# Kernel optimization log

Measured on AMD Instinct MI355X. Metric: run time of the kernel, lower is better.

Reference implementation:

```python
import jax, jax.numpy as jnp
import numpy as np

DOWN = 4
FOCAL_A, FOCAL_B = 2.0, 4.0
RAD_ALPHA = 0.54
HM_W, WH_W = 1.0, 0.1
B, NUM_CLASSES, H, W = 16, 80, 128, 128
MAX_OBJ, N_VALID = 100, 60


def setup_inputs() -> dict:
    key = jax.random.key(0)
    k1, k2, k3, k4, k5, k6, k7, k8 = jax.random.split(key, 8)
    heatmap_heads = jax.random.normal(k1, (B, NUM_CLASSES, H, W), dtype=jnp.float32)
    # wh heads are non-negative distances (l,t,r,b) in input-image pixels
    wh_heads = jax.random.uniform(k2, (B, 4, H, W), dtype=jnp.float32) * 32.0
    # synthetic COCO-style annotations: (x1,y1,x2,y2,cls), cls=-1 pads
    x1 = jax.random.uniform(k3, (B, MAX_OBJ)) * 400.0
    y1 = jax.random.uniform(k4, (B, MAX_OBJ)) * 400.0
    bw = 16.0 + jax.random.uniform(k5, (B, MAX_OBJ)) * 96.0
    bh = 16.0 + jax.random.uniform(k6, (B, MAX_OBJ)) * 96.0
    x2 = jnp.minimum(x1 + bw, 511.0)
    y2 = jnp.minimum(y1 + bh, 511.0)
    cls = jax.random.randint(k7, (B, MAX_OBJ), 0, NUM_CLASSES).astype(jnp.float32)
    cls = jnp.where(jnp.arange(MAX_OBJ)[None, :] < N_VALID, cls, -1.0)
    annotations = jnp.stack([x1, y1, x2, y2, cls], axis=-1).astype(jnp.float32)
    return {"heatmap_heads": heatmap_heads, "wh_heads": wh_heads, "annotations": annotations}


def _single_targets(annots, num_classes, height, width):
    # annots: [N,5]; replicates TTFNet per-image target generation, vectorized.
    boxes = annots[:, :4]
    cls = annots[:, 4]
    valid = cls >= 0
    areas = (boxes[:, 3] - boxes[:, 1] + 1.0) * (boxes[:, 2] - boxes[:, 0] + 1.0)
    log_a = jnp.where(valid, jnp.log(jnp.maximum(areas, 1e-12)), -jnp.inf)
    order = jnp.argsort(-log_a)
    boxes, cls, valid = boxes[order], cls[order], valid[order]
    cx = jnp.trunc((boxes[:, 0] + boxes[:, 2]) * 0.5 / DOWN)
    cy = jnp.trunc((boxes[:, 1] + boxes[:, 3]) * 0.5 / DOWN)
    fx1 = jnp.clip(boxes[:, 0] / DOWN, 0.0, width - 1)
    fx2 = jnp.clip(boxes[:, 2] / DOWN, 0.0, width - 1)
    fy1 = jnp.clip(boxes[:, 1] / DOWN, 0.0, height - 1)
    fy2 = jnp.clip(boxes[:, 3] / DOWN, 0.0, height - 1)
    hr = ((fy2 - fy1) * 0.5 * RAD_ALPHA).astype(jnp.int32)  # .int() trunc (coords >= 0)
    wr = ((fx2 - fx1) * 0.5 * RAD_ALPHA).astype(jnp.int32)
    sx = (2 * wr + 1).astype(jnp.float32) / 6.0  # sigma_x = w/6
    sy = (2 * hr + 1).astype(jnp.float32) / 6.0  # sigma_y = h/6
    xs = jnp.arange(width, dtype=jnp.float32)
    ys = jnp.arange(height, dtype=jnp.float32)
    dx = xs[None, :] - cx[:, None]  # [N,W]
    dy = ys[None, :] - cy[:, None]  # [N,H]
    gx = jnp.where((jnp.abs(dx) <= wr[:, None]) & valid[:, None],
                   jnp.exp(-(dx * dx) / (2.0 * sx[:, None] * sx[:, None])), 0.0)
    gy = jnp.where(jnp.abs(dy) <= hr[:, None],
                   jnp.exp(-(dy * dy) / (2.0 * sy[:, None] * sy[:, None])), 0.0)
    g = gy[:, :, None] * gx[:, None, :]  # [N,H,W] truncated gaussian per box
    cls_idx = jnp.clip(cls.astype(jnp.int32), 0, num_classes - 1)
    hm = jnp.zeros((num_classes, height, width), jnp.float32).at[cls_idx].max(g)
    n = g.shape[0]
    idx = jnp.arange(n)[:, None, None]
    owner = jnp.max(jnp.where(g > 0, idx, -1), axis=0)  # last (smallest) box covering each pixel
    covered = owner >= 0
    oc = jnp.clip(owner, 0)
    box_t = jnp.where(covered[None], jnp.transpose(boxes[oc], (2, 0, 1)), -1.0)  # [4,H,W]
    gsum = jnp.maximum(g.sum(axis=(1, 2)), 1e-12)
    wnorm = g / gsum[:, None, None]  # local_heatmap / ct_div (boxes_area_topk_log is forced to 1.0)
    reg = jnp.where(covered, jnp.take_along_axis(wnorm, oc[None], axis=0)[0], 0.0)[None]  # [1,H,W]
    return hm, box_t, reg


def _forward(heatmap_heads, wh_heads, annotations):
    b, num_classes, height, width = heatmap_heads.shape
    hm_t, box_t, reg_w = jax.vmap(lambda a: _single_targets(a, num_classes, height, width))(annotations)
    hm_t = jax.lax.stop_gradient(hm_t)
    box_t = jax.lax.stop_gradient(box_t)
    reg_w = jax.lax.stop_gradient(reg_w)

    pred = jax.nn.sigmoid(heatmap_heads).transpose(0, 2, 3, 1).reshape(b, -1, num_classes)
    wh = wh_heads.transpose(0, 2, 3, 1).reshape(b, -1, 4)
    tgt = hm_t.transpose(0, 2, 3, 1).reshape(b, -1, num_classes)
    boxes = box_t.transpose(0, 2, 3, 1).reshape(b, -1, 4)
    w = reg_w.transpose(0, 2, 3, 1).reshape(b, -1)

    # focal (CornerNet-style) heatmap loss
    pos = (tgt == 1.0).astype(jnp.float32)
    neg = (tgt < 1.0).astype(jnp.float32)
    neg_wt = (1.0 - tgt) ** FOCAL_B
    pos_loss = jnp.sum(-jnp.log(pred) * (1.0 - pred) ** FOCAL_A * pos)
    neg_loss = jnp.sum(-jnp.log(1.0 - pred) * pred ** FOCAL_A * neg_wt * neg)
    num_pos = pos.sum()
    hm_loss = jnp.where(num_pos > 0, (pos_loss + neg_loss) / num_pos, neg_loss) * HM_W

    # decode predicted boxes on feature grid (stride = down_ratio)
    shift_y, shift_x = jnp.meshgrid(jnp.arange(height, dtype=jnp.float32) * DOWN,
                                    jnp.arange(width, dtype=jnp.float32) * DOWN, indexing='ij')
    base = jnp.stack([shift_x, shift_y], axis=-1).reshape(-1, 2)  # [HW,2]
    pred_boxes = jnp.concatenate([base[None] - wh[:, :, :2], base[None] + wh[:, :, 2:]], axis=2)

    avg_factor = w.sum() + 1e-4
    m = w > 0
    safe = jnp.array([0.0, 0.0, 1.0, 1.0], jnp.float32)
    p = jnp.where(m[..., None], pred_boxes, safe)
    t = jnp.where(m[..., None], boxes, safe)
    lt = jnp.maximum(p[..., :2], t[..., :2])
    rb = jnp.minimum(p[..., 2:], t[..., 2:])
    wh_i = jnp.clip(rb - lt + 1.0, 0.0)
    e1 = jnp.minimum(p[..., :2], t[..., :2])
    e2 = jnp.maximum(p[..., 2:], t[..., 2:])
    ewh = jnp.clip(e2 - e1 + 1.0, 0.0)
    overlap = wh_i[..., 0] * wh_i[..., 1]
    ap = (p[..., 2] - p[..., 0] + 1.0) * (p[..., 3] - p[..., 1] + 1.0)
    ag = (t[..., 2] - t[..., 0] + 1.0) * (t[..., 3] - t[..., 1] + 1.0)
    u = ap + ag - overlap
    ious = overlap / u
    e_area = ewh[..., 0] * ewh[..., 1]
    gious = ious - (e_area - u) / e_area
    wh_loss = (jnp.sum((1.0 - gious) * w) / avg_factor)[None] * WH_W
    return hm_loss, wh_loss


def reference(heatmap_heads, wh_heads, annotations):
    return _forward(heatmap_heads, wh_heads, annotations)
```

## Files before the change

kernel.cpp:

```cpp
#include <hip/hip_runtime.h>
#include <math.h>

#define NB 16
#define NC 80
#define HH 128
#define WW 128
#define NOBJ 100
#define HW (HH*WW)
#define DENSE_BLOCKS 1280
#define TOTAL_BLOCKS (DENSE_BLOCKS + NB*NOBJ)

enum { P_CX=0, P_CY, P_WR, P_HR, P_IVX, P_IVY, P_IVG, P_X1, P_Y1, P_X2, P_Y2, P_CLS, NPAR };

#define ACC_DOUBLES 96
#define NV_OFF 768
#define PAR_OFF 832

__global__ __launch_bounds__(128) void prep_kernel(const float* __restrict__ ann,
                                                   double* __restrict__ acc,
                                                   int* __restrict__ nv,
                                                   float* __restrict__ par) {
    int b = blockIdx.x;
    int i = threadIdx.x;
    __shared__ float skey[128];
    __shared__ int s_nv;
    if (i == 0) s_nv = 0;

    if (i < 5) acc[i * 16 + b] = 0.0;
    if (i == 5) acc[80 + b] = 0.0;

    float x1=0.f, y1=0.f, x2=0.f, y2=0.f, clsv=-1.f;
    float key = INFINITY;
    if (i < NOBJ) {
        const float* a = ann + ((size_t)b * NOBJ + i) * 5;
        x1=a[0]; y1=a[1]; x2=a[2]; y2=a[3]; clsv=a[4];
        if (clsv >= 0.f) {
            float area = (y2 - y1 + 1.f) * (x2 - x1 + 1.f);
            key = -__logf(fmaxf(area, 1e-12f));
        }
    }
    skey[i] = key;
    __syncthreads();

    if (i < NOBJ) {
        int r = 0;
        for (int j = 0; j < NOBJ; ++j) {
            float kj = skey[j];
            if (kj < key || (kj == key && j < i)) r++;
        }
        bool valid = (clsv >= 0.f);
        if (valid) atomicAdd(&s_nv, 1);

        float cx = truncf((x1 + x2) * 0.125f);
        float cy = truncf((y1 + y2) * 0.125f);
        float fx1 = fminf(fmaxf(x1*0.25f, 0.f), WW - 1.f);
        float fx2 = fminf(fmaxf(x2*0.25f, 0.f), WW - 1.f);
        float fy1 = fminf(fmaxf(y1*0.25f, 0.f), HH - 1.f);
        float fy2 = fminf(fmaxf(y2*0.25f, 0.f), HH - 1.f);
        int hr = (int)((fy2 - fy1) * 0.5f * 0.54f);
        int wr = (int)((fx2 - fx1) * 0.5f * 0.54f);
        float sx = (float)(2*wr + 1) / 6.0f;
        float sy = (float)(2*hr + 1) / 6.0f;
        float ivx = 1.f / (2.f * sx * sx);
        float ivy = 1.f / (2.f * sy * sy);

        int yc = (int)cy, xc = (int)cx;
        float sgy = 0.f;
        {
            int ya = max(0, yc - hr), yb = min(HH - 1, yc + hr);
            for (int y = ya; y <= yb; ++y) {
                float dy = (float)y - cy;
                sgy += __expf(-(dy*dy) * ivy);
            }
        }
        float sgx = 0.f;
        if (valid) {
            int xa = max(0, xc - wr), xb = min(WW - 1, xc + wr);
            for (int x = xa; x <= xb; ++x) {
                float dx = (float)x - cx;
                sgx += __expf(-(dx*dx) * ivx);
            }
        }
        float gsum = fmaxf(sgy * sgx, 1e-12f);
        int cls_i = min(max((int)clsv, 0), NC - 1);

        size_t o = (size_t)b * NOBJ + (size_t)r;
        size_t S = (size_t)NB * NOBJ;
        par[P_CX*S + o]  = cx;
        par[P_CY*S + o]  = cy;
        par[P_WR*S + o]  = (float)wr;
        par[P_HR*S + o]  = (float)hr;
        par[P_IVX*S + o] = ivx;
        par[P_IVY*S + o] = ivy;
        par[P_IVG*S + o] = 1.f / gsum;
        par[P_X1*S + o]  = x1;
        par[P_Y1*S + o]  = y1;
        par[P_X2*S + o]  = x2;
        par[P_Y2*S + o]  = y2;
        par[P_CLS*S + o] = __int_as_float(cls_i);
    }
    __syncthreads();
    if (i == 0) nv[b] = s_nv;
}

__global__ __launch_bounds__(256) void main_kernel(const float* __restrict__ heat,
                                                   const float* __restrict__ wh,
                                                   const float* __restrict__ par,
                                                   const int* __restrict__ nv,
                                                   double* __restrict__ acc) {
    if (blockIdx.x < DENSE_BLOCKS) {
        const float4* hp = (const float4*)heat;
        size_t base = (size_t)blockIdx.x * 4096 + threadIdx.x;
        float4 v[16];
        #pragma unroll
        for (int k = 0; k < 16; ++k) v[k] = hp[base + (size_t)k * 256];
        float negl = 0.f;
        #pragma unroll
        for (int k = 0; k < 16; ++k) {
            float hv[4] = { v[k].x, v[k].y, v[k].z, v[k].w };
            #pragma unroll
            for (int m = 0; m < 4; ++m) {
                float h = hv[m];
                float e = __expf(-h);
                float q = 1.f + e;
                float lq = __logf(q);
                float p = 1.f / q;
                negl += (h + lq) * p * p;
            }
        }
        float r = negl;
        for (int off = 32; off > 0; off >>= 1) r += __shfl_down(r, off, 64);
        __shared__ float dred[4];
        int lane = threadIdx.x & 63, wv = threadIdx.x >> 6;
        if (lane == 0) dred[wv] = r;
        __syncthreads();
        if (threadIdx.x == 0) {
            double s = (double)dred[0] + (double)dred[1] + (double)dred[2] + (double)dred[3];
            atomicAdd(&acc[80 + (blockIdx.x & 15)], s);
        }
        return;
    }

    int s = blockIdx.x - DENSE_BLOCKS;
    int b = s / NOBJ;
    int i = s - b * NOBJ;

    __shared__ float sl[NPAR][NOBJ];
    {
        size_t S = (size_t)NB * NOBJ;
        for (int t = threadIdx.x; t < NPAR * NOBJ; t += 256) {
            int pidx = t / NOBJ, o = t - pidx * NOBJ;
            sl[pidx][o] = par[(size_t)pidx * S + (size_t)b * NOBJ + o];
        }
    }
    __syncthreads();
    int nvb = nv[b];
    if (i >= nvb) return;

    float cx = sl[P_CX][i], cy = sl[P_CY][i];
    int wr = (int)sl[P_WR][i], hr = (int)sl[P_HR][i];
    float ivx = sl[P_IVX][i], ivy = sl[P_IVY][i];
    int ci = __float_as_int(sl[P_CLS][i]);
    int xc = (int)cx, yc = (int)cy;
    int xa = max(0, xc - wr), xb = min(WW - 1, xc + wr);
    int ya = max(0, yc - hr), yb = min(HH - 1, yc + hr);
    int wN = xb - xa + 1, hN = yb - ya + 1, npix = wN * hN;

    float posl = 0.f, negl = 0.f, npos = 0.f, wsum = 0.f, gl = 0.f;

    for (int t0 = threadIdx.x; t0 < npix; t0 += 256) {
        int ry = t0 / wN;
        int px = xa + (t0 - ry * wN);
        int py = ya + ry;
        float fx = (float)px, fy = (float)py;

        bool first = true;
        for (int j = 0; j < i; ++j) {
            if (__float_as_int(sl[P_CLS][j]) != ci) continue;
            float dxj = fx - sl[P_CX][j], dyj = fy - sl[P_CY][j];
            if (fabsf(dxj) <= sl[P_WR][j] && fabsf(dyj) <= sl[P_HR][j]) { first = false; break; }
        }

        float dxi = fx - cx, dyi = fy - cy;
        float gi = __expf(-(dxi*dxi) * ivx) * __expf(-(dyi*dyi) * ivy);
        float t = gi;
        bool is_owner = true;
        for (int j = i + 1; j < nvb; ++j) {
            float dxj = fx - sl[P_CX][j], dyj = fy - sl[P_CY][j];
            if (fabsf(dxj) <= sl[P_WR][j] && fabsf(dyj) <= sl[P_HR][j]) {
                is_owner = false;
                if (first && __float_as_int(sl[P_CLS][j]) == ci) {
                    float gj = __expf(-(dxj*dxj) * sl[P_IVX][j]) * __expf(-(dyj*dyj) * sl[P_IVY][j]);
                    t = fmaxf(t, gj);
                }
            }
        }

        if (first) {
            float h = heat[((size_t)b * NC + ci) * HW + (size_t)py * WW + px];
            float e = __expf(-h);
            float q = 1.f + e;
            float lq = __logf(q);
            float p = 1.f / q;
            float basef = (h + lq) * p * p;
            if (t == 1.0f) {
                posl += lq * (1.f - p) * (1.f - p);
                negl -= basef;
                npos += 1.f;
            } else {
                float u1 = 1.f - t;
                float u2 = u1 * u1;
                negl += basef * (u2 * u2 - 1.f);
            }
        }

        if (is_owner) {
            float w = gi * sl[P_IVG][i];
            size_t po = (size_t)py * WW + px;
            const float* whb = wh + (size_t)b * 4 * HW + po;
            float w0 = whb[0], w1 = whb[HW], w2 = whb[2*HW], w3 = whb[3*HW];
            float bx = fx * 4.f, by = fy * 4.f;
            float px1 = bx - w0, py1 = by - w1, px2 = bx + w2, py2 = by + w3;
            float tx1 = sl[P_X1][i], ty1 = sl[P_Y1][i];
            float tx2 = sl[P_X2][i], ty2 = sl[P_Y2][i];
            float ltx = fmaxf(px1, tx1), lty = fmaxf(py1, ty1);
            float rbx = fminf(px2, tx2), rby = fminf(py2, ty2);
            float iw = fmaxf(rbx - ltx + 1.f, 0.f), ih = fmaxf(rby - lty + 1.f, 0.f);
            float e1x = fminf(px1, tx1), e1y = fminf(py1, ty1);
            float e2x = fmaxf(px2, tx2), e2y = fmaxf(py2, ty2);
            float ew = fmaxf(e2x - e1x + 1.f, 0.f), eh = fmaxf(e2y - e1y + 1.f, 0.f);
            float ov = iw * ih;
            float ap = (px2 - px1 + 1.f) * (py2 - py1 + 1.f);
            float ag = (tx2 - tx1 + 1.f) * (ty2 - ty1 + 1.f);
            float u = ap + ag - ov;
            float iou = ov / u;
            float ea = ew * eh;
            float giou = iou - (ea - u) / ea;
            wsum += w;
            gl += (1.f - giou) * w;
        }
    }

    float vals[5] = { posl, negl, npos, wsum, gl };
    #pragma unroll
    for (int k = 0; k < 5; ++k) {
        float v = vals[k];
        for (int off = 32; off > 0; off >>= 1) v += __shfl_down(v, off, 64);
        vals[k] = v;
    }
    __shared__ float red[5][4];
    int lane = threadIdx.x & 63, wv = threadIdx.x >> 6;
    if (lane == 0) {
        #pragma unroll
        for (int k = 0; k < 5; ++k) red[k][wv] = vals[k];
    }
    __syncthreads();
    if (threadIdx.x == 0) {
        #pragma unroll
        for (int k = 0; k < 5; ++k) {
            double vsum = (double)red[k][0] + (double)red[k][1] + (double)red[k][2] + (double)red[k][3];
            atomicAdd(&acc[k * 16 + b], vsum);
        }
    }
}

__global__ void finalize_kernel(const double* __restrict__ acc, float* __restrict__ out) {
    double posl=0, negc=0, npos=0, wsum=0, gl=0, dneg=0;
    for (int b = 0; b < NB; ++b) {
        posl += acc[0*16 + b];
        negc += acc[1*16 + b];
        npos += acc[2*16 + b];
        wsum += acc[3*16 + b];
        gl   += acc[4*16 + b];
        dneg += acc[80 + b];
    }
    double neg = negc + dneg;
    double hm = (npos > 0.0) ? (posl + neg) / npos : neg;
    out[0] = (float)hm;
    out[1] = (float)(gl / (wsum + 1e-4) * 0.1);
}

extern "C" void kernel_launch(void* const* d_in, const int* in_sizes, int n_in,
                              void* d_out, int out_size, void* d_ws, size_t ws_size,
                              hipStream_t stream) {
    const float* heat = (const float*)d_in[0];
    const float* wh   = (const float*)d_in[1];
    const float* ann  = (const float*)d_in[2];
    float* out = (float*)d_out;

    double* acc = (double*)d_ws;
    int*    nv  = (int*)((char*)d_ws + NV_OFF);
    float*  par = (float*)((char*)d_ws + PAR_OFF);

    prep_kernel<<<NB, 128, 0, stream>>>(ann, acc, nv, par);
    main_kernel<<<TOTAL_BLOCKS, 256, 0, stream>>>(heat, wh, par, nv, acc);
    finalize_kernel<<<1, 1, 0, stream>>>(acc, out);
}
```

Before: 146.3 us.

## Schedule scatter blocks first, pack object params as float4, shrink dense blocks

Per-object scatter blocks now come first in the grid, so the long, irregular object blocks start early instead of trailing behind the dense heatmap sweep. Object parameters are stored as three float4 records per object rather than twelve separate planes, and invalid objects now exit before the shared-memory load. Dense blocks process half as many float4 values each, use two partial accumulators, and spread their atomics over 64 double slots instead of 16. The price is twice as many dense blocks and a larger accumulator area in the finalize step.

```diff
diff --git a/kernel.cpp b/kernel.cpp
--- a/kernel.cpp
+++ b/kernel.cpp
@@ -7,19 +7,20 @@
 #define WW 128
 #define NOBJ 100
 #define HW (HH*WW)
-#define DENSE_BLOCKS 1280
-#define TOTAL_BLOCKS (DENSE_BLOCKS + NB*NOBJ)
-
-enum { P_CX=0, P_CY, P_WR, P_HR, P_IVX, P_IVY, P_IVG, P_X1, P_Y1, P_X2, P_Y2, P_CLS, NPAR };
-
-#define ACC_DOUBLES 96
-#define NV_OFF 768
-#define PAR_OFF 832
+#define SCATTER_BLOCKS (NB*NOBJ)
+#define F4_TOTAL (NB*NC*HW/4)
+#define F4_PER_BLOCK (256*8)
+#define DENSE_BLOCKS (F4_TOTAL/F4_PER_BLOCK)
+#define TOTAL_BLOCKS (SCATTER_BLOCKS + DENSE_BLOCKS)
+#define DENSE_SLOTS 64
+
+#define NV_OFF 1152
+#define PAR_OFF 1216
 
 __global__ __launch_bounds__(128) void prep_kernel(const float* __restrict__ ann,
                                                    double* __restrict__ acc,
                                                    int* __restrict__ nv,
-                                                   float* __restrict__ par) {
+                                                   float4* __restrict__ par) {
     int b = blockIdx.x;
     int i = threadIdx.x;
     __shared__ float skey[128];
@@ -27,7 +28,7 @@
     if (i == 0) s_nv = 0;
 
     if (i < 5) acc[i * 16 + b] = 0.0;
-    if (i == 5) acc[80 + b] = 0.0;
+    if (i >= 8 && i < 12) acc[80 + b * 4 + (i - 8)] = 0.0;
 
     float x1=0.f, y1=0.f, x2=0.f, y2=0.f, clsv=-1.f;
     float key = INFINITY;
@@ -84,20 +85,10 @@
         float gsum = fmaxf(sgy * sgx, 1e-12f);
         int cls_i = min(max((int)clsv, 0), NC - 1);
 
-        size_t o = (size_t)b * NOBJ + (size_t)r;
-        size_t S = (size_t)NB * NOBJ;
-        par[P_CX*S + o]  = cx;
-        par[P_CY*S + o]  = cy;
-        par[P_WR*S + o]  = (float)wr;
-        par[P_HR*S + o]  = (float)hr;
-        par[P_IVX*S + o] = ivx;
-        par[P_IVY*S + o] = ivy;
-        par[P_IVG*S + o] = 1.f / gsum;
-        par[P_X1*S + o]  = x1;
-        par[P_Y1*S + o]  = y1;
-        par[P_X2*S + o]  = x2;
-        par[P_Y2*S + o]  = y2;
-        par[P_CLS*S + o] = __int_as_float(cls_i);
+        size_t o = ((size_t)b * NOBJ + (size_t)r) * 3;
+        par[o + 0] = make_float4(cx, cy, (float)wr, (float)hr);
+        par[o + 1] = make_float4(ivx, ivy, __int_as_float(cls_i), 1.f / gsum);
+        par[o + 2] = make_float4(x1, y1, x2, y2);
     }
     __syncthreads();
     if (i == 0) nv[b] = s_nv;
@@ -105,18 +96,19 @@
 
 __global__ __launch_bounds__(256) void main_kernel(const float* __restrict__ heat,
                                                    const float* __restrict__ wh,
-                                                   const float* __restrict__ par,
+                                                   const float4* __restrict__ par,
                                                    const int* __restrict__ nv,
                                                    double* __restrict__ acc) {
-    if (blockIdx.x < DENSE_BLOCKS) {
+    if (blockIdx.x >= SCATTER_BLOCKS) {
+        int db = blockIdx.x - SCATTER_BLOCKS;
         const float4* hp = (const float4*)heat;
-        size_t base = (size_t)blockIdx.x * 4096 + threadIdx.x;
-        float4 v[16];
-        #pragma unroll
-        for (int k = 0; k < 16; ++k) v[k] = hp[base + (size_t)k * 256];
-        float negl = 0.f;
-        #pragma unroll
-        for (int k = 0; k < 16; ++k) {
+        size_t base = (size_t)db * F4_PER_BLOCK + threadIdx.x;
+        float4 v[8];
+        #pragma unroll
+        for (int k = 0; k < 8; ++k) v[k] = hp[base + (size_t)k * 256];
+        float n0 = 0.f, n1 = 0.f;
+        #pragma unroll
+        for (int k = 0; k < 8; ++k) {
             float hv[4] = { v[k].x, v[k].y, v[k].z, v[k].w };
             #pragma unroll
             for (int m = 0; m < 4; ++m) {
@@ -125,10 +117,11 @@
                 float q = 1.f + e;
                 float lq = __logf(q);
                 float p = 1.f / q;
-                negl += (h + lq) * p * p;
-            }
-        }
-        float r = negl;
+                float t = (h + lq) * p * p;
+                if (m & 1) n1 += t; else n0 += t;
+            }
+        }
+        float r = n0 + n1;
         for (int off = 32; off > 0; off >>= 1) r += __shfl_down(r, off, 64);
         __shared__ float dred[4];
         int lane = threadIdx.x & 63, wv = threadIdx.x >> 6;
@@ -136,31 +129,31 @@
         __syncthreads();
         if (threadIdx.x == 0) {
             double s = (double)dred[0] + (double)dred[1] + (double)dred[2] + (double)dred[3];
-            atomicAdd(&acc[80 + (blockIdx.x & 15)], s);
+            atomicAdd(&acc[80 + (db & (DENSE_SLOTS - 1))], s);
         }
         return;
     }
 
-    int s = blockIdx.x - DENSE_BLOCKS;
+    int s = blockIdx.x;
     int b = s / NOBJ;
     int i = s - b * NOBJ;
-
-    __shared__ float sl[NPAR][NOBJ];
-    {
-        size_t S = (size_t)NB * NOBJ;
-        for (int t = threadIdx.x; t < NPAR * NOBJ; t += 256) {
-            int pidx = t / NOBJ, o = t - pidx * NOBJ;
-            sl[pidx][o] = par[(size_t)pidx * S + (size_t)b * NOBJ + o];
-        }
-    }
-    __syncthreads();
     int nvb = nv[b];
     if (i >= nvb) return;
 
-    float cx = sl[P_CX][i], cy = sl[P_CY][i];
-    int wr = (int)sl[P_WR][i], hr = (int)sl[P_HR][i];
-    float ivx = sl[P_IVX][i], ivy = sl[P_IVY][i];
-    int ci = __float_as_int(sl[P_CLS][i]);
+    __shared__ float4 sobj[NOBJ][3];
+    {
+        const float4* src = par + (size_t)b * NOBJ * 3;
+        float4* dst = &sobj[0][0];
+        for (int t = threadIdx.x; t < NOBJ * 3; t += 256) dst[t] = src[t];
+    }
+    __syncthreads();
+
+    float4 g0i = sobj[i][0], g1i = sobj[i][1], g2i = sobj[i][2];
+    float cx = g0i.x, cy = g0i.y;
+    int wr = (int)g0i.z, hr = (int)g0i.w;
+    float ivx = g1i.x, ivy = g1i.y;
+    int ci = __float_as_int(g1i.z);
+    float ivg = g1i.w;
     int xc = (int)cx, yc = (int)cy;
     int xa = max(0, xc - wr), xb = min(WW - 1, xc + wr);
     int ya = max(0, yc - hr), yb = min(HH - 1, yc + hr);
@@ -176,9 +169,10 @@
 
         bool first = true;
         for (int j = 0; j < i; ++j) {
-            if (__float_as_int(sl[P_CLS][j]) != ci) continue;
-            float dxj = fx - sl[P_CX][j], dyj = fy - sl[P_CY][j];
-            if (fabsf(dxj) <= sl[P_WR][j] && fabsf(dyj) <= sl[P_HR][j]) { first = false; break; }
+            float4 g1 = sobj[j][1];
+            if (__float_as_int(g1.z) != ci) continue;
+            float4 g0 = sobj[j][0];
+            if (fabsf(fx - g0.x) <= g0.z && fabsf(fy - g0.y) <= g0.w) { first = false; break; }
         }
 
         float dxi = fx - cx, dyi = fy - cy;
@@ -186,12 +180,16 @@
         float t = gi;
         bool is_owner = true;
         for (int j = i + 1; j < nvb; ++j) {
-            float dxj = fx - sl[P_CX][j], dyj = fy - sl[P_CY][j];
-            if (fabsf(dxj) <= sl[P_WR][j] && fabsf(dyj) <= sl[P_HR][j]) {
+            float4 g0 = sobj[j][0];
+            float dxj = fx - g0.x, dyj = fy - g0.y;
+            if (fabsf(dxj) <= g0.z && fabsf(dyj) <= g0.w) {
                 is_owner = false;
-                if (first && __float_as_int(sl[P_CLS][j]) == ci) {
-                    float gj = __expf(-(dxj*dxj) * sl[P_IVX][j]) * __expf(-(dyj*dyj) * sl[P_IVY][j]);
-                    t = fmaxf(t, gj);
+                if (first) {
+                    float4 g1 = sobj[j][1];
+                    if (__float_as_int(g1.z) == ci) {
+                        float gj = __expf(-(dxj*dxj) * g1.x) * __expf(-(dyj*dyj) * g1.y);
+                        t = fmaxf(t, gj);
+                    }
                 }
             }
         }
@@ -215,14 +213,13 @@
         }
 
         if (is_owner) {
-            float w = gi * sl[P_IVG][i];
+            float w = gi * ivg;
             size_t po = (size_t)py * WW + px;
             const float* whb = wh + (size_t)b * 4 * HW + po;
             float w0 = whb[0], w1 = whb[HW], w2 = whb[2*HW], w3 = whb[3*HW];
             float bx = fx * 4.f, by = fy * 4.f;
             float px1 = bx - w0, py1 = by - w1, px2 = bx + w2, py2 = by + w3;
-            float tx1 = sl[P_X1][i], ty1 = sl[P_Y1][i];
-            float tx2 = sl[P_X2][i], ty2 = sl[P_Y2][i];
+            float tx1 = g2i.x, ty1 = g2i.y, tx2 = g2i.z, ty2 = g2i.w;
             float ltx = fmaxf(px1, tx1), lty = fmaxf(py1, ty1);
             float rbx = fminf(px2, tx2), rby = fminf(py2, ty2);
             float iw = fmaxf(rbx - ltx + 1.f, 0.f), ih = fmaxf(rby - lty + 1.f, 0.f);
@@ -272,8 +269,8 @@
         npos += acc[2*16 + b];
         wsum += acc[3*16 + b];
         gl   += acc[4*16 + b];
-        dneg += acc[80 + b];
-    }
+    }
+    for (int k = 0; k < DENSE_SLOTS; ++k) dneg += acc[80 + k];
     double neg = negc + dneg;
     double hm = (npos > 0.0) ? (posl + neg) / npos : neg;
     out[0] = (float)hm;
@@ -290,7 +287,7 @@
 
     double* acc = (double*)d_ws;
     int*    nv  = (int*)((char*)d_ws + NV_OFF);
-    float*  par = (float*)((char*)d_ws + PAR_OFF);
+    float4* par = (float4*)((char*)d_ws + PAR_OFF);
 
     prep_kernel<<<NB, 128, 0, stream>>>(ann, acc, nv, par);
     main_kernel<<<TOTAL_BLOCKS, 256, 0, stream>>>(heat, wh, par, nv, acc);
```

Result: faster. 141.2 us (-3.5%).
